# Optimization experiments

Hardware: AMD Instinct MI355X
Metric: run time of the kernel (lower is better)

Reference implementation:

```python
import jax, jax.numpy as jnp
import numpy as np

K = 16                 # k nearest neighbors
POS_LO, POS_HI = 0, 3  # position_slice
INF = jnp.float32(1e30)


def setup_inputs() -> dict:
    key = jax.random.key(0)
    k1, k2, k3 = jax.random.split(key, 3)
    B, N, F = 16, 2048, 128
    nodes = jax.random.normal(k1, (B, N, F), dtype=jnp.float32)
    T = jax.random.randint(k2, (B,), 0, 1024)
    taus = jax.random.randint(k3, (B,), 0, 1024)
    return {"nodes": nodes, "T": T, "taus": taus, "B": B}


def reference(nodes, T, taus, B):
    # Faithful, vectorized version of the per-batch causal KNN edge builder.
    # Original: for each batch b, sinks = pos[b, T[b]:T[b]+taus[b]],
    # sources = pos[b, :T[b]+taus[b]]; knn(source, sink, k) returns
    # (sink_local_idx, source_idx); keep edges where sink_local > source;
    # assemble COO adjacency (b, sink_local, source) with weight 1.
    # Here we return the equivalent DENSE [B, N, N] adjacency.
    pos = nodes[:, :, POS_LO:POS_HI]              # [B, N, d]
    N = pos.shape[1]
    i_idx = jnp.arange(N)                         # local sink index grid
    # global index of sink i in batch b is T[b] + i
    sink_gidx = jnp.clip(T[:, None] + i_idx[None, :], 0, N - 1)   # [B, N]
    sink_pos = jnp.take_along_axis(pos, sink_gidx[..., None], axis=1)  # [B, N, d]
    sink_valid = i_idx[None, :] < taus[:, None]                    # [B, N]
    src_valid = i_idx[None, :] < (T + taus)[:, None]               # [B, N]
    # squared distances sink->source: [B, N_sink, N_src]
    d2 = jnp.sum((sink_pos[:, :, None, :] - pos[:, None, :, :]) ** 2, axis=-1)
    d2 = jnp.where(src_valid[:, None, :], d2, INF)
    neg_vals, nbr = jax.lax.top_k(-d2, K)          # k smallest distances, [B, N, K]
    nbr_valid = neg_vals > -INF                    # source actually existed
    causal = i_idx[None, :, None] > nbr            # edge[0] > edge[1] mask (local sink idx)
    valid = sink_valid[:, :, None] & nbr_valid & causal
    adj = jnp.zeros((B, N, N), dtype=jnp.float32)
    b_idx = jnp.arange(B)[:, None, None]
    adj = adj.at[b_idx, i_idx[None, :, None], nbr].add(
        jnp.where(valid, jnp.float32(1.0), jnp.float32(0.0)))
    return adj
```

## Files before the change

kernel.cpp:

```cpp
#include <hip/hip_runtime.h>

#define NN 2048
#define FF 128
#define KK 16
#define INF_KEY 0xFFFFFFFFFFFFFFFFull

__device__ __forceinline__ unsigned wave_min_u32(unsigned x) {
    int v = (int)x, t;
    t = __builtin_amdgcn_update_dpp(v, v, 0x111, 0xf, 0xf, false);
    v = ((unsigned)t < (unsigned)v) ? t : v;
    t = __builtin_amdgcn_update_dpp(v, v, 0x112, 0xf, 0xf, false);
    v = ((unsigned)t < (unsigned)v) ? t : v;
    t = __builtin_amdgcn_update_dpp(v, v, 0x114, 0xf, 0xf, false);
    v = ((unsigned)t < (unsigned)v) ? t : v;
    t = __builtin_amdgcn_update_dpp(v, v, 0x118, 0xf, 0xf, false);
    v = ((unsigned)t < (unsigned)v) ? t : v;
    t = __builtin_amdgcn_update_dpp(v, v, 0x142, 0xf, 0xf, false);
    v = ((unsigned)t < (unsigned)v) ? t : v;
    t = __builtin_amdgcn_update_dpp(v, v, 0x143, 0xf, 0xf, false);
    v = ((unsigned)t < (unsigned)v) ? t : v;
    return (unsigned)__builtin_amdgcn_readlane(v, 63);
}

__global__ __launch_bounds__(256) void knn_adj_fused(
    const float* __restrict__ nodes,
    const int*   __restrict__ T_arr,
    const int*   __restrict__ tau_arr,
    float*       __restrict__ adj)
{
    const int b    = blockIdx.x;
    const int i0   = blockIdx.y << 2;
    const int tid  = threadIdx.x;
    const int wave = tid >> 6;
    const int lane = tid & 63;

    const int tau = tau_arr[b];
    float* block_out = adj + ((size_t)b * NN + i0) * NN;

    if (i0 >= tau) {
        const float4 z = make_float4(0.f, 0.f, 0.f, 0.f);
        float4* out4 = (float4*)block_out;
        #pragma unroll
        for (int t = 0; t < 8; ++t)
            out4[tid + (t << 8)] = z;
        return;
    }

    const int T = T_arr[b];
    const int M = T + tau;

    __shared__ float sx[NN], sy[NN], sz[NN];
    __shared__ unsigned swords[4][64];
    for (int j = tid; j < M; j += 256) {
        const float* p = nodes + ((size_t)b * NN + j) * FF;
        sx[j] = p[0];
        sy[j] = p[1];
        sz[j] = p[2];
    }
    __syncthreads();

    const int i = i0 + wave;
    float4* out4 = (float4*)(block_out + (size_t)wave * NN);

    if (i >= tau) {
        const float4 z = make_float4(0.f, 0.f, 0.f, 0.f);
        #pragma unroll
        for (int t = 0; t < 8; ++t)
            out4[(t << 6) + lane] = z;
        return;
    }

    const int g = T + i;
    const float sxv = sx[g], syv = sy[g], szv = sz[g];

    unsigned long long q0 = INF_KEY, q1 = INF_KEY, q2 = INF_KEY, q3 = INF_KEY;
    const int S = (M + 63) >> 6;
    #pragma unroll 4
    for (int s = 0; s < S; ++s) {
        const int j = lane + (s << 6);
        if (j < M) {
            float dx = __fsub_rn(sxv, sx[j]);
            float dy = __fsub_rn(syv, sy[j]);
            float dz = __fsub_rn(szv, sz[j]);
            float d2 = __fadd_rn(__fadd_rn(__fmul_rn(dx, dx), __fmul_rn(dy, dy)),
                                 __fmul_rn(dz, dz));
            unsigned long long key =
                ((unsigned long long)__float_as_uint(d2) << 32) | (unsigned)(j + 1);
            if (key < q3) {
                q3 = key;
                unsigned long long t;
                if (q3 < q2) { t = q2; q2 = q3; q3 = t; }
                if (q2 < q1) { t = q1; q1 = q2; q2 = t; }
                if (q1 < q0) { t = q0; q0 = q1; q1 = t; }
            }
        }
    }

    unsigned colmask = 0;
    unsigned long long lastpop = 0;
    for (int k = 0; k < KK; ++k) {
        const unsigned hd = (unsigned)(q0 >> 32);
        const unsigned m  = wave_min_u32(hd);
        if (m == 0xFFFFFFFFu) break;

        const unsigned long long mask = __ballot(hd == m);
        unsigned jwin;
        if (__popcll(mask) == 1) {
            const int w = __builtin_ctzll(mask);
            jwin = (unsigned)__builtin_amdgcn_readlane((int)(unsigned)q0, w);
        } else {
            unsigned jc = (hd == m) ? (unsigned)q0 : 0xFFFFFFFFu;
            jwin = wave_min_u32(jc);
        }
        const int j = (int)jwin - 1;

        if (j < i && (j >> 5) == lane)
            colmask |= 1u << (j & 31);

        if (hd == m && (unsigned)q0 == jwin) {
            lastpop = ((unsigned long long)m << 32) | jwin;
            q0 = q1; q1 = q2; q2 = q3; q3 = INF_KEY;
            if (q0 == INF_KEY) {
                unsigned long long best = INF_KEY;
                for (int s2 = 0; s2 < S; ++s2) {
                    const int jj = lane + (s2 << 6);
                    if (jj < M) {
                        float dx = __fsub_rn(sxv, sx[jj]);
                        float dy = __fsub_rn(syv, sy[jj]);
                        float dz = __fsub_rn(szv, sz[jj]);
                        float d2 = __fadd_rn(
                            __fadd_rn(__fmul_rn(dx, dx), __fmul_rn(dy, dy)),
                            __fmul_rn(dz, dz));
                        unsigned long long kk =
                            ((unsigned long long)__float_as_uint(d2) << 32)
                            | (unsigned)(jj + 1);
                        if (kk > lastpop && kk < best) best = kk;
                    }
                }
                q0 = best;
            }
        }
    }

    swords[wave][lane] = colmask;
    #pragma unroll
    for (int k = 0; k < 8; ++k) {
        const unsigned w   = swords[wave][(k << 3) + (lane >> 3)];
        const unsigned nib = (w >> ((lane & 7) << 2)) & 0xFu;
        float4 v;
        v.x = (nib & 1u) ? 1.0f : 0.0f;
        v.y = (nib & 2u) ? 1.0f : 0.0f;
        v.z = (nib & 4u) ? 1.0f : 0.0f;
        v.w = (nib & 8u) ? 1.0f : 0.0f;
        out4[(k << 6) + lane] = v;
    }
}

extern "C" void kernel_launch(void* const* d_in, const int* in_sizes, int n_in,
                              void* d_out, int out_size, void* d_ws, size_t ws_size,
                              hipStream_t stream) {
    const float* nodes = (const float*)d_in[0];
    const int*   T     = (const int*)d_in[1];
    const int*   taus  = (const int*)d_in[2];
    float*       adj   = (float*)d_out;
    const int B = in_sizes[1];

    dim3 grid(B, NN / 4);
    knn_adj_fused<<<grid, dim3(256), 0, stream>>>(nodes, T, taus, adj);
}
```

Baseline: 276.4 us.

## Pack xyz in a pre-pass and read it via cache, drop LDS staging

Adds a pre-kernel that packs each node's xyz into a float4 workspace buffer. The main kernel then reads positions straight from global memory (cache-resident) instead of staging all M positions into 24KB of LDS with a block-wide sync. This removes the per-block strided gather of nodes and the shared-memory limit on occupancy, and the launch bounds now request 8 blocks per CU. Output writes switch to nontemporal stores. The costs are an extra kernel launch and per-lane global/L2 loads in the inner loop and in the rescan path instead of LDS reads.

```diff
diff --git a/kernel.cpp b/kernel.cpp
--- a/kernel.cpp
+++ b/kernel.cpp
@@ -5,6 +5,8 @@
 #define KK 16
 #define INF_KEY 0xFFFFFFFFFFFFFFFFull
 
+typedef float f32x4 __attribute__((ext_vector_type(4)));
+
 __device__ __forceinline__ unsigned wave_min_u32(unsigned x) {
     int v = (int)x, t;
     t = __builtin_amdgcn_update_dpp(v, v, 0x111, 0xf, 0xf, false);
@@ -22,8 +24,29 @@
     return (unsigned)__builtin_amdgcn_readlane(v, 63);
 }
 
-__global__ __launch_bounds__(256) void knn_adj_fused(
-    const float* __restrict__ nodes,
+__global__ __launch_bounds__(256) void pack_xyz(
+    const float* __restrict__ nodes, f32x4* __restrict__ out, int total)
+{
+    const int t = blockIdx.x * 256 + threadIdx.x;
+    if (t < total) {
+        const float* p = nodes + (size_t)t * FF;
+        out[t] = (f32x4){p[0], p[1], p[2], 0.f};
+    }
+}
+
+template<bool PACKED>
+__device__ __forceinline__ f32x4 load_xyz(const float* __restrict__ base, int idx) {
+    if constexpr (PACKED) {
+        return ((const f32x4*)base)[idx];
+    } else {
+        const float* p = base + (size_t)idx * FF;
+        return (f32x4){p[0], p[1], p[2], 0.f};
+    }
+}
+
+template<bool PACKED>
+__global__ __launch_bounds__(256, 8) void knn_adj_fused(
+    const float* __restrict__ xyz,
     const int*   __restrict__ T_arr,
     const int*   __restrict__ tau_arr,
     float*       __restrict__ adj)
@@ -38,40 +61,34 @@
     float* block_out = adj + ((size_t)b * NN + i0) * NN;
 
     if (i0 >= tau) {
-        const float4 z = make_float4(0.f, 0.f, 0.f, 0.f);
-        float4* out4 = (float4*)block_out;
+        const f32x4 z = (f32x4){0.f, 0.f, 0.f, 0.f};
+        f32x4* out4 = (f32x4*)block_out;
         #pragma unroll
         for (int t = 0; t < 8; ++t)
-            out4[tid + (t << 8)] = z;
+            __builtin_nontemporal_store(z, &out4[tid + (t << 8)]);
+        return;
+    }
+
+    const int i = i0 + wave;
+    f32x4* out4 = (f32x4*)(block_out + (size_t)wave * NN);
+
+    if (i >= tau) {
+        const f32x4 z = (f32x4){0.f, 0.f, 0.f, 0.f};
+        #pragma unroll
+        for (int t = 0; t < 8; ++t)
+            __builtin_nontemporal_store(z, &out4[(t << 6) + lane]);
         return;
     }
 
     const int T = T_arr[b];
     const int M = T + tau;
-
-    __shared__ float sx[NN], sy[NN], sz[NN];
+    const float* base = PACKED ? xyz + (size_t)b * NN * 4
+                               : xyz + (size_t)b * NN * FF;
     __shared__ unsigned swords[4][64];
-    for (int j = tid; j < M; j += 256) {
-        const float* p = nodes + ((size_t)b * NN + j) * FF;
-        sx[j] = p[0];
-        sy[j] = p[1];
-        sz[j] = p[2];
-    }
-    __syncthreads();
-
-    const int i = i0 + wave;
-    float4* out4 = (float4*)(block_out + (size_t)wave * NN);
-
-    if (i >= tau) {
-        const float4 z = make_float4(0.f, 0.f, 0.f, 0.f);
-        #pragma unroll
-        for (int t = 0; t < 8; ++t)
-            out4[(t << 6) + lane] = z;
-        return;
-    }
 
     const int g = T + i;
-    const float sxv = sx[g], syv = sy[g], szv = sz[g];
+    const f32x4 sp = load_xyz<PACKED>(base, g);
+    const float sxv = sp.x, syv = sp.y, szv = sp.z;
 
     unsigned long long q0 = INF_KEY, q1 = INF_KEY, q2 = INF_KEY, q3 = INF_KEY;
     const int S = (M + 63) >> 6;
@@ -79,9 +96,10 @@
     for (int s = 0; s < S; ++s) {
         const int j = lane + (s << 6);
         if (j < M) {
-            float dx = __fsub_rn(sxv, sx[j]);
-            float dy = __fsub_rn(syv, sy[j]);
-            float dz = __fsub_rn(szv, sz[j]);
+            const f32x4 v = load_xyz<PACKED>(base, j);
+            float dx = __fsub_rn(sxv, v.x);
+            float dy = __fsub_rn(syv, v.y);
+            float dz = __fsub_rn(szv, v.z);
             float d2 = __fadd_rn(__fadd_rn(__fmul_rn(dx, dx), __fmul_rn(dy, dy)),
                                  __fmul_rn(dz, dz));
             unsigned long long key =
@@ -125,9 +143,10 @@
                 for (int s2 = 0; s2 < S; ++s2) {
                     const int jj = lane + (s2 << 6);
                     if (jj < M) {
-                        float dx = __fsub_rn(sxv, sx[jj]);
-                        float dy = __fsub_rn(syv, sy[jj]);
-                        float dz = __fsub_rn(szv, sz[jj]);
+                        const f32x4 v = load_xyz<PACKED>(base, jj);
+                        float dx = __fsub_rn(sxv, v.x);
+                        float dy = __fsub_rn(syv, v.y);
+                        float dz = __fsub_rn(szv, v.z);
                         float d2 = __fadd_rn(
                             __fadd_rn(__fmul_rn(dx, dx), __fmul_rn(dy, dy)),
                             __fmul_rn(dz, dz));
@@ -147,12 +166,12 @@
     for (int k = 0; k < 8; ++k) {
         const unsigned w   = swords[wave][(k << 3) + (lane >> 3)];
         const unsigned nib = (w >> ((lane & 7) << 2)) & 0xFu;
-        float4 v;
+        f32x4 v;
         v.x = (nib & 1u) ? 1.0f : 0.0f;
         v.y = (nib & 2u) ? 1.0f : 0.0f;
         v.z = (nib & 4u) ? 1.0f : 0.0f;
         v.w = (nib & 8u) ? 1.0f : 0.0f;
-        out4[(k << 6) + lane] = v;
+        __builtin_nontemporal_store(v, &out4[(k << 6) + lane]);
     }
 }
 
@@ -166,5 +185,16 @@
     const int B = in_sizes[1];
 
     dim3 grid(B, NN / 4);
-    knn_adj_fused<<<grid, dim3(256), 0, stream>>>(nodes, T, taus, adj);
-}
+    const size_t need = (size_t)B * NN * sizeof(f32x4);
+
+    if (d_ws != nullptr && ws_size >= need) {
+        const int total = B * NN;
+        pack_xyz<<<dim3((total + 255) / 256), dim3(256), 0, stream>>>(
+            nodes, (f32x4*)d_ws, total);
+        knn_adj_fused<true><<<grid, dim3(256), 0, stream>>>(
+            (const float*)d_ws, T, taus, adj);
+    } else {
+        knn_adj_fused<false><<<grid, dim3(256), 0, stream>>>(
+            nodes, T, taus, adj);
+    }
+}
```

Result: slower. 286.9 us (+3.8%).
